# Kernel optimization log

Hardware: AMD Instinct MI355X
Metric: run time of the kernel (lower is better)

Reference implementation:

```python
import jax, jax.numpy as jnp
import numpy as np

B, N, P_EDGE = 2048, 64, 0.08


def setup_inputs() -> dict:
    key = jax.random.key(0)
    k1, _ = jax.random.split(key)
    u = jax.random.uniform(k1, (B, N, N))
    upper = jnp.triu(u < P_EDGE, k=1)
    A = (upper | jnp.swapaxes(upper, -1, -2)).astype(jnp.float32)  # symmetric, zero diag
    E = jnp.stack([1.0 - A, A], axis=-1)  # [B,N,N,2] one-hot edges
    node_mask = jnp.ones((B, N), dtype=jnp.float32)
    return {"E": E, "node_mask": node_mask}


def _diag(X):
    return jnp.diagonal(X, axis1=-2, axis2=-1)


def _trace(X):
    return _diag(X).sum(-1)


def reference(E, node_mask):
    A = E[..., 1:].sum(-1).astype(jnp.float32)  # [B,N,N]
    d = A.sum(-1)                               # degrees [B,N]
    k2 = A @ A
    k3 = k2 @ A
    k4 = k3 @ A
    k5 = k4 @ A
    k6 = k5 @ A

    c3 = _diag(k3)
    k3x = (c3 / 2)[..., None]
    k3y = (c3.sum(-1) / 6)[..., None]

    diag_a4 = _diag(k4)
    c4 = diag_a4 - d * (d - 1) - jnp.einsum('bij,bj->bi', A, d)
    k4x = (c4 / 2)[..., None]
    k4y = (c4.sum(-1) / 8)[..., None]

    diag_a5 = _diag(k5)
    tri = c3
    c5 = diag_a5 - 2 * tri * d - jnp.einsum('bij,bj->bi', A, tri) + tri
    k5x = (c5 / 2)[..., None]
    k5y = (c5.sum(-1) / 10)[..., None]

    t1 = _trace(k6)
    t2 = _trace(k3 ** 2)
    t3 = jnp.sum(A * k2 ** 2, axis=(-2, -1))
    d2 = _diag(k2)
    t4 = (d2 * diag_a4).sum(-1)
    t5 = _trace(k4)
    t6 = _trace(k3)
    t7 = (d2 ** 3).sum(-1)
    t8 = jnp.sum(k3, axis=(-2, -1))
    t9 = (d2 ** 2).sum(-1)
    t10 = _trace(k2)
    c6 = t1 - 3 * t2 + 9 * t3 - 6 * t4 + 6 * t5 - 4 * t6 + 4 * t7 + 3 * t8 - 12 * t9 + 4 * t10
    k6y = (c6 / 12)[..., None]

    x_cycles = jnp.concatenate([k3x, k4x, k5x], axis=-1)            # [B,N,3]
    y_cycles = jnp.concatenate([k3y, k4y, k5y, k6y], axis=-1)       # [B,4]

    x_cycles = x_cycles * node_mask[..., None] / 10.0
    y_cycles = y_cycles / 10.0
    x_cycles = jnp.minimum(x_cycles, 1.0)
    y_cycles = jnp.minimum(y_cycles, 1.0)
    return x_cycles, y_cycles
```

## Files before the change

### kernel.cpp

```cpp
#include <hip/hip_runtime.h>


typedef __attribute__((ext_vector_type(8))) short bf16x8;
typedef __attribute__((ext_vector_type(16))) float f32x16;

constexpr int BATCH = 2048;
constexpr int NN = 64;

__device__ __forceinline__ bf16x8 frag_ld(const unsigned short* buf, int row, int kb2) {
  const int idx = row * 64 + ((kb2 ^ (row & 7)) << 3);
  const uint4 v = *reinterpret_cast<const uint4*>(buf + idx);
  union { uint4 u; bf16x8 b; } cv; cv.u = v; return cv.b;
}

__global__ __launch_bounds__(256, 8) void node_cycle_kernel(
    const float4* __restrict__ E4,
    const float* __restrict__ nmask,
    float* __restrict__ out)
{
  const int b = blockIdx.x;
  const int tid = threadIdx.x;
  const int lane = tid & 63;
  const int w = tid >> 6;
  const int h = lane >> 5;
  const int c31 = lane & 31;
  const int R = w >> 1, C = w & 1;

  __shared__ unsigned short bufA[64 * 64];
  __shared__ unsigned short bufK2[64 * 64];
  __shared__ unsigned short sl[4][64];
  __shared__ uint2 rms[NN];
  __shared__ float c3sh[NN];
  __shared__ float4 gpart[4];

  const float4* __restrict__ Eb = E4 + (size_t)b * (NN * NN / 2);

  const int rp_r = 16 * w + (lane >> 2);
  const int rp_q = lane & 3;
  const float m_r = nmask[b * NN + rp_r];

  unsigned mA = 0u, mB = 0u;
  #pragma unroll
  for (int q = 0; q < 8; ++q) {
    const float4 f = Eb[w * 512 + q * 64 + lane];
    const int bit = 2 * q + h;
    mA |= (unsigned)(f.y > 0.5f) << bit;
    mB |= (unsigned)(f.w > 0.5f) << bit;
  }
  mA |= (unsigned)__shfl_xor((int)mA, 32);
  mB |= (unsigned)__shfl_xor((int)mB, 32);
  if (lane < 32) {
    sl[w][2 * lane]     = (unsigned short)mA;
    sl[w][2 * lane + 1] = (unsigned short)mB;
  }
  __syncthreads();

  if (tid < 128) {
    const int c = tid >> 1, hf = tid & 1;
    const unsigned v = (unsigned)sl[2 * hf][c] | ((unsigned)sl[2 * hf + 1][c] << 16);
    if (hf == 0) rms[c].x = v; else rms[c].y = v;
  }
  __syncthreads();

  const uint2 mrL = rms[lane];

  {
    const unsigned word = (w < 2) ? mrL.x : mrL.y;
    const unsigned bits16 = (word >> (16 * (w & 1))) & 0xffffu;
    #pragma unroll
    for (int e = 0; e < 2; ++e) {
      const int bq = 2 * w + e;
      unsigned wv[4];
      #pragma unroll
      for (int p2 = 0; p2 < 4; ++p2) {
        const int c0 = e * 8 + p2 * 2;
        wv[p2] = (((bits16 >> c0) & 1u) ? 0x3F80u : 0u)
               | (((bits16 >> (c0 + 1)) & 1u) ? 0x3F800000u : 0u);
      }
      const int idx = lane * 64 + ((bq ^ (lane & 7)) << 3);
      *reinterpret_cast<uint4*>(&bufA[idx]) = make_uint4(wv[0], wv[1], wv[2], wv[3]);
    }
  }
  __syncthreads();

  bf16x8 Bf[4];
  #pragma unroll
  for (int K = 0; K < 4; ++K) Bf[K] = frag_ld(bufA, C * 32 + c31, 2 * K + h);

  f32x16 acc;
  #pragma unroll
  for (int r = 0; r < 16; ++r) acc[r] = 0.f;
  #pragma unroll
  for (int K = 0; K < 4; ++K) {
    const bf16x8 af = frag_ld(bufA, R * 32 + c31, 2 * K + h);
    acc = __builtin_amdgcn_mfma_f32_32x32x16_bf16(af, Bf[K], acc, 0, 0, 0);
  }

  {
    const int c = C * 32 + c31;
    #pragma unroll
    for (int g = 0; g < 4; ++g) {
      const unsigned w0 = (__float_as_uint(acc[4*g+1]) & 0xffff0000u) |
                          (__float_as_uint(acc[4*g+0]) >> 16);
      const unsigned w1 = (__float_as_uint(acc[4*g+3]) & 0xffff0000u) |
                          (__float_as_uint(acc[4*g+2]) >> 16);
      const int bb = (4 * R + g) ^ (c & 7);
      *reinterpret_cast<uint2*>(&bufK2[c * 64 + bb * 8 + h * 4]) = make_uint2(w0, w1);
    }
  }
  __syncthreads();

  f32x16 d;
  #pragma unroll
  for (int r = 0; r < 16; ++r) d[r] = 0.f;
  #pragma unroll
  for (int K = 0; K < 4; ++K) {
    const bf16x8 kf = frag_ld(bufK2, R * 32 + c31, 2 * K + h);
    d = __builtin_amdgcn_mfma_f32_32x32x16_bf16(kf, Bf[K], d, 0, 0, 0);
  }

  if (R == C) {
    const int dtarget = c31 - 4 * h;
    float c3d = 0.f;
    #pragma unroll
    for (int r = 0; r < 16; ++r) {
      const int rowbase = (r & 3) + 8 * (r >> 2);
      c3d += (rowbase == dtarget) ? d[r] : 0.f;
    }
    if (((c31 >> 2) & 1) == h) c3sh[R * 32 + c31] = c3d;
  }

  {
    const int c = C * 32 + c31;
    #pragma unroll
    for (int g = 0; g < 4; ++g) {
      const unsigned u0 = ((unsigned)d[4*g+0]) | (((unsigned)d[4*g+1]) << 16);
      const unsigned u1 = ((unsigned)d[4*g+2]) | (((unsigned)d[4*g+3]) << 16);
      const int bb = (4 * R + g) ^ (c & 7);
      *reinterpret_cast<uint2*>(&bufA[c * 64 + bb * 8 + h * 4]) = make_uint2(u0, u1);
    }
  }
  __syncthreads();

  const uint2 mr = rms[rp_r];
  float diag4 = 0.f, Ad = 0.f, diag5 = 0.f, t3p = 0.f, Atri = 0.f;
  float t1p = 0.f, t8p = 0.f;
  #pragma unroll
  for (int e = 0; e < 2; ++e) {
    const int bq = 2 * rp_q + e;
    const int idx = rp_r * 64 + ((bq ^ (rp_r & 7)) << 3);
    const uint4 vk2 = *reinterpret_cast<const uint4*>(&bufK2[idx]);
    const uint4 vk3 = *reinterpret_cast<const uint4*>(&bufA[idx]);
    const float4 c3a = *reinterpret_cast<const float4*>(&c3sh[bq * 8]);
    const float4 c3b = *reinterpret_cast<const float4*>(&c3sh[bq * 8 + 4]);
    const unsigned wk2[4] = {vk2.x, vk2.y, vk2.z, vk2.w};
    const unsigned wk3[4] = {vk3.x, vk3.y, vk3.z, vk3.w};
    const float c3v[8] = {c3a.x, c3a.y, c3a.z, c3a.w, c3b.x, c3b.y, c3b.z, c3b.w};
    #pragma unroll
    for (int e2 = 0; e2 < 4; ++e2) {
      const int j0 = bq * 8 + 2 * e2;
      const float k2lo = __uint_as_float(wk2[e2] << 16);
      const float k2hi = __uint_as_float(wk2[e2] & 0xffff0000u);
      const float k3lo = (float)(wk3[e2] & 0xffffu);
      const float k3hi = (float)(wk3[e2] >> 16);
      diag4 = fmaf(k2lo, k2lo, fmaf(k2hi, k2hi, diag4));
      Ad += k2lo + k2hi;
      diag5 = fmaf(k2lo, k3lo, fmaf(k2hi, k3hi, diag5));
      t1p = fmaf(k3lo, k3lo, fmaf(k3hi, k3hi, t1p));
      t8p += k3lo + k3hi;
      const unsigned b0 = (j0 < 32 ? (mr.x >> j0) : (mr.y >> (j0 - 32))) & 1u;
      const unsigned b1 = ((j0 + 1) < 32 ? (mr.x >> (j0 + 1)) : (mr.y >> (j0 + 1 - 32))) & 1u;
      t3p = fmaf(b0 ? k2lo : 0.f, k2lo, fmaf(b1 ? k2hi : 0.f, k2hi, t3p));
      Atri += (b0 ? c3v[2 * e2] : 0.f) + (b1 ? c3v[2 * e2 + 1] : 0.f);
    }
  }
  #pragma unroll
  for (int off = 1; off <= 2; off <<= 1) {
    diag4 += __shfl_xor(diag4, off);
    Ad    += __shfl_xor(Ad, off);
    diag5 += __shfl_xor(diag5, off);
    t3p   += __shfl_xor(t3p, off);
    Atri  += __shfl_xor(Atri, off);
    t1p   += __shfl_xor(t1p, off);
    t8p   += __shfl_xor(t8p, off);
  }

  const float di  = (float)(__popc(mr.x) + __popc(mr.y));
  const float c3i = c3sh[rp_r];
  const float c4 = diag4 - di * (di - 1.f) - Ad;
  const float c5 = diag5 - 2.f * c3i * di - Atri + c3i;
  const float c6p = t1p + 3.f * t8p
            - 3.f * (c3i * c3i)
            + 9.f * t3p
            - 6.f * (di * diag4)
            + 6.f * diag4
            - 4.f * c3i
            + 4.f * (di * di * di)
            - 12.f * (di * di)
            + 4.f * di;

  if (rp_q == 0) {
    float* xo = out + ((size_t)b * NN + rp_r) * 3;
    xo[0] = fminf(c3i * 0.05f * m_r, 1.f);
    xo[1] = fminf(c4  * 0.05f * m_r, 1.f);
    xo[2] = fminf(c5  * 0.05f * m_r, 1.f);
  }

  float sc3 = c3i, sc4 = c4, sc5 = c5, sc6 = c6p;
  #pragma unroll
  for (int off = 4; off < 64; off <<= 1) {
    sc3 += __shfl_xor(sc3, off);
    sc4 += __shfl_xor(sc4, off);
    sc5 += __shfl_xor(sc5, off);
    sc6 += __shfl_xor(sc6, off);
  }
  if (lane == 0) gpart[w] = make_float4(sc3, sc4, sc5, sc6);
  __syncthreads();

  if (tid == 0) {
    const float4 g0 = gpart[0], g1 = gpart[1], g2 = gpart[2], g3 = gpart[3];
    float4 y;
    y.x = fminf((g0.x + g1.x + g2.x + g3.x) * (1.f / 6.f)  * 0.1f, 1.f);
    y.y = fminf((g0.y + g1.y + g2.y + g3.y) * (1.f / 8.f)  * 0.1f, 1.f);
    y.z = fminf((g0.z + g1.z + g2.z + g3.z) * (1.f / 10.f) * 0.1f, 1.f);
    y.w = fminf((g0.w + g1.w + g2.w + g3.w) * (1.f / 12.f) * 0.1f, 1.f);
    *reinterpret_cast<float4*>(out + (size_t)BATCH * NN * 3 + b * 4) = y;
  }
}

extern "C" void kernel_launch(void* const* d_in, const int* in_sizes, int n_in,
                              void* d_out, int out_size, void* d_ws, size_t ws_size,
                              hipStream_t stream) {
  const float4* E4 = reinterpret_cast<const float4*>(d_in[0]);
  const float* nmask = reinterpret_cast<const float*>(d_in[1]);
  float* out = reinterpret_cast<float*>(d_out);
  node_cycle_kernel<<<BATCH, 256, 0, stream>>>(E4, nmask, out);
}
```

Baseline: 18.81 us.

## Process two graphs per workgroup to interleave independent work and amortize barriers

Each 256-thread block now handles two batch elements instead of one. The mask build, MFMA products, packing and row passes for both graphs are interleaved between shared barriers. The goal is more instruction-level parallelism per wave, overlapping the two graphs' global loads and MFMA latency, and fewer barriers per graph. In exchange the block uses twice the LDS and more registers, occupancy is lowered to 4 blocks per CU, and the grid is halved.

```diff
diff --git a/kernel.cpp b/kernel.cpp
--- a/kernel.cpp
+++ b/kernel.cpp
@@ -13,32 +13,9 @@
   union { uint4 u; bf16x8 b; } cv; cv.u = v; return cv.b;
 }
 
-__global__ __launch_bounds__(256, 8) void node_cycle_kernel(
-    const float4* __restrict__ E4,
-    const float* __restrict__ nmask,
-    float* __restrict__ out)
-{
-  const int b = blockIdx.x;
-  const int tid = threadIdx.x;
-  const int lane = tid & 63;
-  const int w = tid >> 6;
-  const int h = lane >> 5;
-  const int c31 = lane & 31;
-  const int R = w >> 1, C = w & 1;
-
-  __shared__ unsigned short bufA[64 * 64];
-  __shared__ unsigned short bufK2[64 * 64];
-  __shared__ unsigned short sl[4][64];
-  __shared__ uint2 rms[NN];
-  __shared__ float c3sh[NN];
-  __shared__ float4 gpart[4];
-
-  const float4* __restrict__ Eb = E4 + (size_t)b * (NN * NN / 2);
-
-  const int rp_r = 16 * w + (lane >> 2);
-  const int rp_q = lane & 3;
-  const float m_r = nmask[b * NN + rp_r];
-
+__device__ __forceinline__ void build_masks(const float4* __restrict__ Eb,
+                                            int w, int lane, int h,
+                                            unsigned short (*slw)[64]) {
   unsigned mA = 0u, mB = 0u;
   #pragma unroll
   for (int q = 0; q < 8; ++q) {
@@ -50,75 +27,70 @@
   mA |= (unsigned)__shfl_xor((int)mA, 32);
   mB |= (unsigned)__shfl_xor((int)mB, 32);
   if (lane < 32) {
-    sl[w][2 * lane]     = (unsigned short)mA;
-    sl[w][2 * lane + 1] = (unsigned short)mB;
-  }
-  __syncthreads();
-
-  if (tid < 128) {
-    const int c = tid >> 1, hf = tid & 1;
-    const unsigned v = (unsigned)sl[2 * hf][c] | ((unsigned)sl[2 * hf + 1][c] << 16);
-    if (hf == 0) rms[c].x = v; else rms[c].y = v;
-  }
-  __syncthreads();
-
-  const uint2 mrL = rms[lane];
-
-  {
-    const unsigned word = (w < 2) ? mrL.x : mrL.y;
-    const unsigned bits16 = (word >> (16 * (w & 1))) & 0xffffu;
+    slw[w][2 * lane]     = (unsigned short)mA;
+    slw[w][2 * lane + 1] = (unsigned short)mB;
+  }
+}
+
+__device__ __forceinline__ void write_A(unsigned short* bA, uint2 mm, int w, int lane) {
+  const unsigned word = (w < 2) ? mm.x : mm.y;
+  const unsigned bits16 = (word >> (16 * (w & 1))) & 0xffffu;
+  #pragma unroll
+  for (int e = 0; e < 2; ++e) {
+    const int bq = 2 * w + e;
+    unsigned wv[4];
     #pragma unroll
-    for (int e = 0; e < 2; ++e) {
-      const int bq = 2 * w + e;
-      unsigned wv[4];
-      #pragma unroll
-      for (int p2 = 0; p2 < 4; ++p2) {
-        const int c0 = e * 8 + p2 * 2;
-        wv[p2] = (((bits16 >> c0) & 1u) ? 0x3F80u : 0u)
-               | (((bits16 >> (c0 + 1)) & 1u) ? 0x3F800000u : 0u);
-      }
-      const int idx = lane * 64 + ((bq ^ (lane & 7)) << 3);
-      *reinterpret_cast<uint4*>(&bufA[idx]) = make_uint4(wv[0], wv[1], wv[2], wv[3]);
+    for (int p2 = 0; p2 < 4; ++p2) {
+      const int c0 = e * 8 + p2 * 2;
+      wv[p2] = (((bits16 >> c0) & 1u) ? 0x3F80u : 0u)
+             | (((bits16 >> (c0 + 1)) & 1u) ? 0x3F800000u : 0u);
     }
-  }
-  __syncthreads();
-
-  bf16x8 Bf[4];
-  #pragma unroll
-  for (int K = 0; K < 4; ++K) Bf[K] = frag_ld(bufA, C * 32 + c31, 2 * K + h);
-
+    const int idx = lane * 64 + ((bq ^ (lane & 7)) << 3);
+    *reinterpret_cast<uint4*>(&bA[idx]) = make_uint4(wv[0], wv[1], wv[2], wv[3]);
+  }
+}
+
+__device__ __forceinline__ f32x16 do_mm(const unsigned short* bufOp, const bf16x8* Bf,
+                                        int R, int c31, int h) {
   f32x16 acc;
   #pragma unroll
   for (int r = 0; r < 16; ++r) acc[r] = 0.f;
   #pragma unroll
   for (int K = 0; K < 4; ++K) {
-    const bf16x8 af = frag_ld(bufA, R * 32 + c31, 2 * K + h);
+    const bf16x8 af = frag_ld(bufOp, R * 32 + c31, 2 * K + h);
     acc = __builtin_amdgcn_mfma_f32_32x32x16_bf16(af, Bf[K], acc, 0, 0, 0);
   }
-
-  {
-    const int c = C * 32 + c31;
-    #pragma unroll
-    for (int g = 0; g < 4; ++g) {
-      const unsigned w0 = (__float_as_uint(acc[4*g+1]) & 0xffff0000u) |
-                          (__float_as_uint(acc[4*g+0]) >> 16);
-      const unsigned w1 = (__float_as_uint(acc[4*g+3]) & 0xffff0000u) |
-                          (__float_as_uint(acc[4*g+2]) >> 16);
-      const int bb = (4 * R + g) ^ (c & 7);
-      *reinterpret_cast<uint2*>(&bufK2[c * 64 + bb * 8 + h * 4]) = make_uint2(w0, w1);
-    }
-  }
-  __syncthreads();
-
-  f32x16 d;
-  #pragma unroll
-  for (int r = 0; r < 16; ++r) d[r] = 0.f;
-  #pragma unroll
-  for (int K = 0; K < 4; ++K) {
-    const bf16x8 kf = frag_ld(bufK2, R * 32 + c31, 2 * K + h);
-    d = __builtin_amdgcn_mfma_f32_32x32x16_bf16(kf, Bf[K], d, 0, 0, 0);
-  }
-
+  return acc;
+}
+
+__device__ __forceinline__ void pack_k2(unsigned short* bK2, const f32x16& acc,
+                                        int R, int C, int c31, int h) {
+  const int c = C * 32 + c31;
+  #pragma unroll
+  for (int g = 0; g < 4; ++g) {
+    const unsigned w0 = (__float_as_uint(acc[4*g+1]) & 0xffff0000u) |
+                        (__float_as_uint(acc[4*g+0]) >> 16);
+    const unsigned w1 = (__float_as_uint(acc[4*g+3]) & 0xffff0000u) |
+                        (__float_as_uint(acc[4*g+2]) >> 16);
+    const int bb = (4 * R + g) ^ (c & 7);
+    *reinterpret_cast<uint2*>(&bK2[c * 64 + bb * 8 + h * 4]) = make_uint2(w0, w1);
+  }
+}
+
+__device__ __forceinline__ void pack_k3(unsigned short* bK3, const f32x16& d,
+                                        int R, int C, int c31, int h) {
+  const int c = C * 32 + c31;
+  #pragma unroll
+  for (int g = 0; g < 4; ++g) {
+    const unsigned u0 = ((unsigned)d[4*g+0]) | (((unsigned)d[4*g+1]) << 16);
+    const unsigned u1 = ((unsigned)d[4*g+2]) | (((unsigned)d[4*g+3]) << 16);
+    const int bb = (4 * R + g) ^ (c & 7);
+    *reinterpret_cast<uint2*>(&bK3[c * 64 + bb * 8 + h * 4]) = make_uint2(u0, u1);
+  }
+}
+
+__device__ __forceinline__ void diag_c3(float* c3p, const f32x16& d,
+                                        int R, int C, int c31, int h) {
   if (R == C) {
     const int dtarget = c31 - 4 * h;
     float c3d = 0.f;
@@ -127,32 +99,23 @@
       const int rowbase = (r & 3) + 8 * (r >> 2);
       c3d += (rowbase == dtarget) ? d[r] : 0.f;
     }
-    if (((c31 >> 2) & 1) == h) c3sh[R * 32 + c31] = c3d;
-  }
-
-  {
-    const int c = C * 32 + c31;
-    #pragma unroll
-    for (int g = 0; g < 4; ++g) {
-      const unsigned u0 = ((unsigned)d[4*g+0]) | (((unsigned)d[4*g+1]) << 16);
-      const unsigned u1 = ((unsigned)d[4*g+2]) | (((unsigned)d[4*g+3]) << 16);
-      const int bb = (4 * R + g) ^ (c & 7);
-      *reinterpret_cast<uint2*>(&bufA[c * 64 + bb * 8 + h * 4]) = make_uint2(u0, u1);
-    }
-  }
-  __syncthreads();
-
-  const uint2 mr = rms[rp_r];
-  float diag4 = 0.f, Ad = 0.f, diag5 = 0.f, t3p = 0.f, Atri = 0.f;
-  float t1p = 0.f, t8p = 0.f;
+    if (((c31 >> 2) & 1) == h) c3p[R * 32 + c31] = c3d;
+  }
+}
+
+struct RP { float diag4, Ad, diag5, t3p, Atri, t1p, t8p; };
+
+__device__ __forceinline__ RP rowpass(const unsigned short* bK2, const unsigned short* bK3,
+                                      const float* c3p, uint2 mr, int rp_r, int rp_q) {
+  RP o = {0.f, 0.f, 0.f, 0.f, 0.f, 0.f, 0.f};
   #pragma unroll
   for (int e = 0; e < 2; ++e) {
     const int bq = 2 * rp_q + e;
     const int idx = rp_r * 64 + ((bq ^ (rp_r & 7)) << 3);
-    const uint4 vk2 = *reinterpret_cast<const uint4*>(&bufK2[idx]);
-    const uint4 vk3 = *reinterpret_cast<const uint4*>(&bufA[idx]);
-    const float4 c3a = *reinterpret_cast<const float4*>(&c3sh[bq * 8]);
-    const float4 c3b = *reinterpret_cast<const float4*>(&c3sh[bq * 8 + 4]);
+    const uint4 vk2 = *reinterpret_cast<const uint4*>(&bK2[idx]);
+    const uint4 vk3 = *reinterpret_cast<const uint4*>(&bK3[idx]);
+    const float4 c3a = *reinterpret_cast<const float4*>(&c3p[bq * 8]);
+    const float4 c3b = *reinterpret_cast<const float4*>(&c3p[bq * 8 + 4]);
     const unsigned wk2[4] = {vk2.x, vk2.y, vk2.z, vk2.w};
     const unsigned wk3[4] = {vk3.x, vk3.y, vk3.z, vk3.w};
     const float c3v[8] = {c3a.x, c3a.y, c3a.z, c3a.w, c3b.x, c3b.y, c3b.z, c3b.w};
@@ -163,44 +126,38 @@
       const float k2hi = __uint_as_float(wk2[e2] & 0xffff0000u);
       const float k3lo = (float)(wk3[e2] & 0xffffu);
       const float k3hi = (float)(wk3[e2] >> 16);
-      diag4 = fmaf(k2lo, k2lo, fmaf(k2hi, k2hi, diag4));
-      Ad += k2lo + k2hi;
-      diag5 = fmaf(k2lo, k3lo, fmaf(k2hi, k3hi, diag5));
-      t1p = fmaf(k3lo, k3lo, fmaf(k3hi, k3hi, t1p));
-      t8p += k3lo + k3hi;
+      o.diag4 = fmaf(k2lo, k2lo, fmaf(k2hi, k2hi, o.diag4));
+      o.Ad += k2lo + k2hi;
+      o.diag5 = fmaf(k2lo, k3lo, fmaf(k2hi, k3hi, o.diag5));
+      o.t1p = fmaf(k3lo, k3lo, fmaf(k3hi, k3hi, o.t1p));
+      o.t8p += k3lo + k3hi;
       const unsigned b0 = (j0 < 32 ? (mr.x >> j0) : (mr.y >> (j0 - 32))) & 1u;
       const unsigned b1 = ((j0 + 1) < 32 ? (mr.x >> (j0 + 1)) : (mr.y >> (j0 + 1 - 32))) & 1u;
-      t3p = fmaf(b0 ? k2lo : 0.f, k2lo, fmaf(b1 ? k2hi : 0.f, k2hi, t3p));
-      Atri += (b0 ? c3v[2 * e2] : 0.f) + (b1 ? c3v[2 * e2 + 1] : 0.f);
+      o.t3p = fmaf(b0 ? k2lo : 0.f, k2lo, fmaf(b1 ? k2hi : 0.f, k2hi, o.t3p));
+      o.Atri += (b0 ? c3v[2 * e2] : 0.f) + (b1 ? c3v[2 * e2 + 1] : 0.f);
     }
   }
-  #pragma unroll
-  for (int off = 1; off <= 2; off <<= 1) {
-    diag4 += __shfl_xor(diag4, off);
-    Ad    += __shfl_xor(Ad, off);
-    diag5 += __shfl_xor(diag5, off);
-    t3p   += __shfl_xor(t3p, off);
-    Atri  += __shfl_xor(Atri, off);
-    t1p   += __shfl_xor(t1p, off);
-    t8p   += __shfl_xor(t8p, off);
-  }
-
-  const float di  = (float)(__popc(mr.x) + __popc(mr.y));
-  const float c3i = c3sh[rp_r];
-  const float c4 = diag4 - di * (di - 1.f) - Ad;
-  const float c5 = diag5 - 2.f * c3i * di - Atri + c3i;
-  const float c6p = t1p + 3.f * t8p
+  return o;
+}
+
+__device__ __forceinline__ void epilogue(const RP& r, uint2 mr, float c3i, float m_r,
+                                         int bb, int rp_r, int rp_q, int lane, int w,
+                                         float* __restrict__ out, float4* gp) {
+  const float di = (float)(__popc(mr.x) + __popc(mr.y));
+  const float c4 = r.diag4 - di * (di - 1.f) - r.Ad;
+  const float c5 = r.diag5 - 2.f * c3i * di - r.Atri + c3i;
+  const float c6p = r.t1p + 3.f * r.t8p
             - 3.f * (c3i * c3i)
-            + 9.f * t3p
-            - 6.f * (di * diag4)
-            + 6.f * diag4
+            + 9.f * r.t3p
+            - 6.f * (di * r.diag4)
+            + 6.f * r.diag4
             - 4.f * c3i
             + 4.f * (di * di * di)
             - 12.f * (di * di)
             + 4.f * di;
 
   if (rp_q == 0) {
-    float* xo = out + ((size_t)b * NN + rp_r) * 3;
+    float* xo = out + ((size_t)bb * NN + rp_r) * 3;
     xo[0] = fminf(c3i * 0.05f * m_r, 1.f);
     xo[1] = fminf(c4  * 0.05f * m_r, 1.f);
     xo[2] = fminf(c5  * 0.05f * m_r, 1.f);
@@ -214,17 +171,102 @@
     sc5 += __shfl_xor(sc5, off);
     sc6 += __shfl_xor(sc6, off);
   }
-  if (lane == 0) gpart[w] = make_float4(sc3, sc4, sc5, sc6);
-  __syncthreads();
-
-  if (tid == 0) {
-    const float4 g0 = gpart[0], g1 = gpart[1], g2 = gpart[2], g3 = gpart[3];
+  if (lane == 0) gp[w] = make_float4(sc3, sc4, sc5, sc6);
+}
+
+__global__ __launch_bounds__(256, 4) void node_cycle_kernel(
+    const float4* __restrict__ E4,
+    const float* __restrict__ nmask,
+    float* __restrict__ out)
+{
+  const int tid = threadIdx.x;
+  const int lane = tid & 63;
+  const int w = tid >> 6;
+  const int h = lane >> 5;
+  const int c31 = lane & 31;
+  const int R = w >> 1, C = w & 1;
+  const int b0 = blockIdx.x * 2;
+
+  __shared__ unsigned short bufA[2][4096];
+  __shared__ unsigned short bufK2[2][4096];
+  __shared__ unsigned short sl[2][4][64];
+  __shared__ uint2 rms[2][NN];
+  __shared__ float c3sh[2][NN];
+  __shared__ float4 gpart[2][4];
+
+  const float4* __restrict__ Eb0 = E4 + (size_t)b0 * 2048;
+  const float4* __restrict__ Eb1 = Eb0 + 2048;
+
+  const int rp_r = 16 * w + (lane >> 2);
+  const int rp_q = lane & 3;
+  const float m_r0 = nmask[(size_t)b0 * NN + rp_r];
+  const float m_r1 = nmask[(size_t)(b0 + 1) * NN + rp_r];
+
+  build_masks(Eb0, w, lane, h, sl[0]);
+  build_masks(Eb1, w, lane, h, sl[1]);
+  __syncthreads();
+
+  {
+    const int bi = tid >> 7;
+    const int t = tid & 127;
+    const int c = t >> 1, hf = t & 1;
+    const unsigned v = (unsigned)sl[bi][2 * hf][c] | ((unsigned)sl[bi][2 * hf + 1][c] << 16);
+    if (hf == 0) rms[bi][c].x = v; else rms[bi][c].y = v;
+  }
+  __syncthreads();
+
+  write_A(bufA[0], rms[0][lane], w, lane);
+  write_A(bufA[1], rms[1][lane], w, lane);
+  __syncthreads();
+
+  bf16x8 Bf0[4], Bf1[4];
+  #pragma unroll
+  for (int K = 0; K < 4; ++K) {
+    Bf0[K] = frag_ld(bufA[0], C * 32 + c31, 2 * K + h);
+    Bf1[K] = frag_ld(bufA[1], C * 32 + c31, 2 * K + h);
+  }
+  const f32x16 acc0 = do_mm(bufA[0], Bf0, R, c31, h);
+  const f32x16 acc1 = do_mm(bufA[1], Bf1, R, c31, h);
+  pack_k2(bufK2[0], acc0, R, C, c31, h);
+  pack_k2(bufK2[1], acc1, R, C, c31, h);
+  __syncthreads();
+
+  const f32x16 d0 = do_mm(bufK2[0], Bf0, R, c31, h);
+  const f32x16 d1 = do_mm(bufK2[1], Bf1, R, c31, h);
+  diag_c3(c3sh[0], d0, R, C, c31, h);
+  diag_c3(c3sh[1], d1, R, C, c31, h);
+  pack_k3(bufA[0], d0, R, C, c31, h);
+  pack_k3(bufA[1], d1, R, C, c31, h);
+  __syncthreads();
+
+  const uint2 mr0 = rms[0][rp_r];
+  const uint2 mr1 = rms[1][rp_r];
+  RP r0 = rowpass(bufK2[0], bufA[0], c3sh[0], mr0, rp_r, rp_q);
+  RP r1 = rowpass(bufK2[1], bufA[1], c3sh[1], mr1, rp_r, rp_q);
+  #pragma unroll
+  for (int off = 1; off <= 2; off <<= 1) {
+    r0.diag4 += __shfl_xor(r0.diag4, off); r1.diag4 += __shfl_xor(r1.diag4, off);
+    r0.Ad    += __shfl_xor(r0.Ad, off);    r1.Ad    += __shfl_xor(r1.Ad, off);
+    r0.diag5 += __shfl_xor(r0.diag5, off); r1.diag5 += __shfl_xor(r1.diag5, off);
+    r0.t3p   += __shfl_xor(r0.t3p, off);   r1.t3p   += __shfl_xor(r1.t3p, off);
+    r0.Atri  += __shfl_xor(r0.Atri, off);  r1.Atri  += __shfl_xor(r1.Atri, off);
+    r0.t1p   += __shfl_xor(r0.t1p, off);   r1.t1p   += __shfl_xor(r1.t1p, off);
+    r0.t8p   += __shfl_xor(r0.t8p, off);   r1.t8p   += __shfl_xor(r1.t8p, off);
+  }
+
+  epilogue(r0, mr0, c3sh[0][rp_r], m_r0, b0,     rp_r, rp_q, lane, w, out, gpart[0]);
+  epilogue(r1, mr1, c3sh[1][rp_r], m_r1, b0 + 1, rp_r, rp_q, lane, w, out, gpart[1]);
+  __syncthreads();
+
+  if (tid < 2) {
+    const float4 g0 = gpart[tid][0], g1 = gpart[tid][1],
+                 g2 = gpart[tid][2], g3 = gpart[tid][3];
     float4 y;
     y.x = fminf((g0.x + g1.x + g2.x + g3.x) * (1.f / 6.f)  * 0.1f, 1.f);
     y.y = fminf((g0.y + g1.y + g2.y + g3.y) * (1.f / 8.f)  * 0.1f, 1.f);
     y.z = fminf((g0.z + g1.z + g2.z + g3.z) * (1.f / 10.f) * 0.1f, 1.f);
     y.w = fminf((g0.w + g1.w + g2.w + g3.w) * (1.f / 12.f) * 0.1f, 1.f);
-    *reinterpret_cast<float4*>(out + (size_t)BATCH * NN * 3 + b * 4) = y;
+    *reinterpret_cast<float4*>(out + (size_t)BATCH * NN * 3 + (b0 + tid) * 4) = y;
   }
 }
 
@@ -234,5 +276,5 @@
   const float4* E4 = reinterpret_cast<const float4*>(d_in[0]);
   const float* nmask = reinterpret_cast<const float*>(d_in[1]);
   float* out = reinterpret_cast<float*>(d_out);
-  node_cycle_kernel<<<BATCH, 256, 0, stream>>>(E4, nmask, out);
-}
+  node_cycle_kernel<<<BATCH / 2, 256, 0, stream>>>(E4, nmask, out);
+}
```

Measured after the change: 21.17 us. +12.6%, slower.

## Split edge-tensor bit packing into a separate pre-pass kernel

Applied to the files above, without the earlier changes.

Moves the conversion of the float one-hot edge tensor into per-row adjacency bitmasks into a separate kernel that writes them to workspace. The main kernel then loads the compact bitmasks instead of streaming the full float input, and its body is refactored into helper functions. An extra sync is added after the second matmul so the K3 result can overwrite the A buffer safely. This adds a second launch and a global round trip of the masks, while the dominant input read is unchanged.

```diff
diff --git a/kernel.cpp b/kernel.cpp
--- a/kernel.cpp
+++ b/kernel.cpp
@@ -13,8 +13,153 @@
   union { uint4 u; bf16x8 b; } cv; cv.u = v; return cv.b;
 }
 
+__global__ __launch_bounds__(256) void pack_kernel(
+    const float4* __restrict__ E4,
+    unsigned* __restrict__ rw)
+{
+  const int b = blockIdx.x;
+  const int tid = threadIdx.x;
+  const int lane = tid & 63;
+  const int w = tid >> 6;
+  const int h = lane >> 5;
+
+  __shared__ unsigned short sl[4][64];
+
+  const float4* __restrict__ Eb = E4 + (size_t)b * 2048;
+  unsigned mA = 0u, mB = 0u;
+  #pragma unroll
+  for (int q = 0; q < 8; ++q) {
+    const float4 f = Eb[w * 512 + q * 64 + lane];
+    const int bit = 2 * q + h;
+    mA |= (unsigned)(f.y > 0.5f) << bit;
+    mB |= (unsigned)(f.w > 0.5f) << bit;
+  }
+  mA |= (unsigned)__shfl_xor((int)mA, 32);
+  mB |= (unsigned)__shfl_xor((int)mB, 32);
+  if (lane < 32) {
+    sl[w][2 * lane]     = (unsigned short)mA;
+    sl[w][2 * lane + 1] = (unsigned short)mB;
+  }
+  __syncthreads();
+
+  if (tid < 128) {
+    const int c = tid >> 1, hf = tid & 1;
+    const unsigned v = (unsigned)sl[2 * hf][c] | ((unsigned)sl[2 * hf + 1][c] << 16);
+    rw[(b * 64 + c) * 2 + hf] = v;
+  }
+}
+
+__device__ __forceinline__ void write_A(unsigned short* bA, uint2 mm, int w, int lane) {
+  const unsigned word = (w < 2) ? mm.x : mm.y;
+  const unsigned bits16 = (word >> (16 * (w & 1))) & 0xffffu;
+  #pragma unroll
+  for (int e = 0; e < 2; ++e) {
+    const int bq = 2 * w + e;
+    unsigned wv[4];
+    #pragma unroll
+    for (int p2 = 0; p2 < 4; ++p2) {
+      const int c0 = e * 8 + p2 * 2;
+      wv[p2] = (((bits16 >> c0) & 1u) ? 0x3F80u : 0u)
+             | (((bits16 >> (c0 + 1)) & 1u) ? 0x3F800000u : 0u);
+    }
+    const int idx = lane * 64 + ((bq ^ (lane & 7)) << 3);
+    *reinterpret_cast<uint4*>(&bA[idx]) = make_uint4(wv[0], wv[1], wv[2], wv[3]);
+  }
+}
+
+__device__ __forceinline__ f32x16 do_mm(const unsigned short* opA, const unsigned short* opB,
+                                        int R, int C, int c31, int h) {
+  f32x16 acc;
+  #pragma unroll
+  for (int r = 0; r < 16; ++r) acc[r] = 0.f;
+  #pragma unroll
+  for (int K = 0; K < 4; ++K) {
+    const bf16x8 af = frag_ld(opA, R * 32 + c31, 2 * K + h);
+    const bf16x8 bf = frag_ld(opB, C * 32 + c31, 2 * K + h);
+    acc = __builtin_amdgcn_mfma_f32_32x32x16_bf16(af, bf, acc, 0, 0, 0);
+  }
+  return acc;
+}
+
+__device__ __forceinline__ void pack_k2(unsigned short* bK2, const f32x16& acc,
+                                        int R, int C, int c31, int h) {
+  const int c = C * 32 + c31;
+  #pragma unroll
+  for (int g = 0; g < 4; ++g) {
+    const unsigned w0 = (__float_as_uint(acc[4*g+1]) & 0xffff0000u) |
+                        (__float_as_uint(acc[4*g+0]) >> 16);
+    const unsigned w1 = (__float_as_uint(acc[4*g+3]) & 0xffff0000u) |
+                        (__float_as_uint(acc[4*g+2]) >> 16);
+    const int bb = (4 * R + g) ^ (c & 7);
+    *reinterpret_cast<uint2*>(&bK2[c * 64 + bb * 8 + h * 4]) = make_uint2(w0, w1);
+  }
+}
+
+__device__ __forceinline__ void pack_k3(unsigned short* bK3, const f32x16& d,
+                                        int R, int C, int c31, int h) {
+  const int c = C * 32 + c31;
+  #pragma unroll
+  for (int g = 0; g < 4; ++g) {
+    const unsigned u0 = ((unsigned)d[4*g+0]) | (((unsigned)d[4*g+1]) << 16);
+    const unsigned u1 = ((unsigned)d[4*g+2]) | (((unsigned)d[4*g+3]) << 16);
+    const int bb = (4 * R + g) ^ (c & 7);
+    *reinterpret_cast<uint2*>(&bK3[c * 64 + bb * 8 + h * 4]) = make_uint2(u0, u1);
+  }
+}
+
+__device__ __forceinline__ void diag_c3(float* c3p, const f32x16& d,
+                                        int R, int C, int c31, int h) {
+  if (R == C) {
+    const int dtarget = c31 - 4 * h;
+    float c3d = 0.f;
+    #pragma unroll
+    for (int r = 0; r < 16; ++r) {
+      const int rowbase = (r & 3) + 8 * (r >> 2);
+      c3d += (rowbase == dtarget) ? d[r] : 0.f;
+    }
+    if (((c31 >> 2) & 1) == h) c3p[R * 32 + c31] = c3d;
+  }
+}
+
+struct RP { float diag4, Ad, diag5, t3p, Atri, t1p, t8p; };
+
+__device__ __forceinline__ RP rowpass(const unsigned short* bK2, const unsigned short* bK3,
+                                      const float* c3p, uint2 mr, int rp_r, int rp_q) {
+  RP o = {0.f, 0.f, 0.f, 0.f, 0.f, 0.f, 0.f};
+  #pragma unroll
+  for (int e = 0; e < 2; ++e) {
+    const int bq = 2 * rp_q + e;
+    const int idx = rp_r * 64 + ((bq ^ (rp_r & 7)) << 3);
+    const uint4 vk2 = *reinterpret_cast<const uint4*>(&bK2[idx]);
+    const uint4 vk3 = *reinterpret_cast<const uint4*>(&bK3[idx]);
+    const float4 c3a = *reinterpret_cast<const float4*>(&c3p[bq * 8]);
+    const float4 c3b = *reinterpret_cast<const float4*>(&c3p[bq * 8 + 4]);
+    const unsigned wk2[4] = {vk2.x, vk2.y, vk2.z, vk2.w};
+    const unsigned wk3[4] = {vk3.x, vk3.y, vk3.z, vk3.w};
+    const float c3v[8] = {c3a.x, c3a.y, c3a.z, c3a.w, c3b.x, c3b.y, c3b.z, c3b.w};
+    #pragma unroll
+    for (int e2 = 0; e2 < 4; ++e2) {
+      const int j0 = bq * 8 + 2 * e2;
+      const float k2lo = __uint_as_float(wk2[e2] << 16);
+      const float k2hi = __uint_as_float(wk2[e2] & 0xffff0000u);
+      const float k3lo = (float)(wk3[e2] & 0xffffu);
+      const float k3hi = (float)(wk3[e2] >> 16);
+      o.diag4 = fmaf(k2lo, k2lo, fmaf(k2hi, k2hi, o.diag4));
+      o.Ad += k2lo + k2hi;
+      o.diag5 = fmaf(k2lo, k3lo, fmaf(k2hi, k3hi, o.diag5));
+      o.t1p = fmaf(k3lo, k3lo, fmaf(k3hi, k3hi, o.t1p));
+      o.t8p += k3lo + k3hi;
+      const unsigned b0 = (j0 < 32 ? (mr.x >> j0) : (mr.y >> (j0 - 32))) & 1u;
+      const unsigned b1 = ((j0 + 1) < 32 ? (mr.x >> (j0 + 1)) : (mr.y >> (j0 + 1 - 32))) & 1u;
+      o.t3p = fmaf(b0 ? k2lo : 0.f, k2lo, fmaf(b1 ? k2hi : 0.f, k2hi, o.t3p));
+      o.Atri += (b0 ? c3v[2 * e2] : 0.f) + (b1 ? c3v[2 * e2 + 1] : 0.f);
+    }
+  }
+  return o;
+}
+
 __global__ __launch_bounds__(256, 8) void node_cycle_kernel(
-    const float4* __restrict__ E4,
+    const uint2* __restrict__ rw,
     const float* __restrict__ nmask,
     float* __restrict__ out)
 {
@@ -26,174 +171,55 @@
   const int c31 = lane & 31;
   const int R = w >> 1, C = w & 1;
 
-  __shared__ unsigned short bufA[64 * 64];
-  __shared__ unsigned short bufK2[64 * 64];
-  __shared__ unsigned short sl[4][64];
+  __shared__ unsigned short bufA[4096];
+  __shared__ unsigned short bufK2[4096];
   __shared__ uint2 rms[NN];
   __shared__ float c3sh[NN];
   __shared__ float4 gpart[4];
 
-  const float4* __restrict__ Eb = E4 + (size_t)b * (NN * NN / 2);
+  if (tid < 64) rms[tid] = rw[b * 64 + tid];
+  __syncthreads();
 
   const int rp_r = 16 * w + (lane >> 2);
   const int rp_q = lane & 3;
   const float m_r = nmask[b * NN + rp_r];
 
-  unsigned mA = 0u, mB = 0u;
-  #pragma unroll
-  for (int q = 0; q < 8; ++q) {
-    const float4 f = Eb[w * 512 + q * 64 + lane];
-    const int bit = 2 * q + h;
-    mA |= (unsigned)(f.y > 0.5f) << bit;
-    mB |= (unsigned)(f.w > 0.5f) << bit;
-  }
-  mA |= (unsigned)__shfl_xor((int)mA, 32);
-  mB |= (unsigned)__shfl_xor((int)mB, 32);
-  if (lane < 32) {
-    sl[w][2 * lane]     = (unsigned short)mA;
-    sl[w][2 * lane + 1] = (unsigned short)mB;
-  }
-  __syncthreads();
-
-  if (tid < 128) {
-    const int c = tid >> 1, hf = tid & 1;
-    const unsigned v = (unsigned)sl[2 * hf][c] | ((unsigned)sl[2 * hf + 1][c] << 16);
-    if (hf == 0) rms[c].x = v; else rms[c].y = v;
-  }
-  __syncthreads();
-
-  const uint2 mrL = rms[lane];
-
-  {
-    const unsigned word = (w < 2) ? mrL.x : mrL.y;
-    const unsigned bits16 = (word >> (16 * (w & 1))) & 0xffffu;
-    #pragma unroll
-    for (int e = 0; e < 2; ++e) {
-      const int bq = 2 * w + e;
-      unsigned wv[4];
-      #pragma unroll
-      for (int p2 = 0; p2 < 4; ++p2) {
-        const int c0 = e * 8 + p2 * 2;
-        wv[p2] = (((bits16 >> c0) & 1u) ? 0x3F80u : 0u)
-               | (((bits16 >> (c0 + 1)) & 1u) ? 0x3F800000u : 0u);
-      }
-      const int idx = lane * 64 + ((bq ^ (lane & 7)) << 3);
-      *reinterpret_cast<uint4*>(&bufA[idx]) = make_uint4(wv[0], wv[1], wv[2], wv[3]);
-    }
-  }
-  __syncthreads();
-
-  bf16x8 Bf[4];
-  #pragma unroll
-  for (int K = 0; K < 4; ++K) Bf[K] = frag_ld(bufA, C * 32 + c31, 2 * K + h);
-
-  f32x16 acc;
-  #pragma unroll
-  for (int r = 0; r < 16; ++r) acc[r] = 0.f;
-  #pragma unroll
-  for (int K = 0; K < 4; ++K) {
-    const bf16x8 af = frag_ld(bufA, R * 32 + c31, 2 * K + h);
-    acc = __builtin_amdgcn_mfma_f32_32x32x16_bf16(af, Bf[K], acc, 0, 0, 0);
-  }
-
-  {
-    const int c = C * 32 + c31;
-    #pragma unroll
-    for (int g = 0; g < 4; ++g) {
-      const unsigned w0 = (__float_as_uint(acc[4*g+1]) & 0xffff0000u) |
-                          (__float_as_uint(acc[4*g+0]) >> 16);
-      const unsigned w1 = (__float_as_uint(acc[4*g+3]) & 0xffff0000u) |
-                          (__float_as_uint(acc[4*g+2]) >> 16);
-      const int bb = (4 * R + g) ^ (c & 7);
-      *reinterpret_cast<uint2*>(&bufK2[c * 64 + bb * 8 + h * 4]) = make_uint2(w0, w1);
-    }
-  }
-  __syncthreads();
-
-  f32x16 d;
-  #pragma unroll
-  for (int r = 0; r < 16; ++r) d[r] = 0.f;
-  #pragma unroll
-  for (int K = 0; K < 4; ++K) {
-    const bf16x8 kf = frag_ld(bufK2, R * 32 + c31, 2 * K + h);
-    d = __builtin_amdgcn_mfma_f32_32x32x16_bf16(kf, Bf[K], d, 0, 0, 0);
-  }
-
-  if (R == C) {
-    const int dtarget = c31 - 4 * h;
-    float c3d = 0.f;
-    #pragma unroll
-    for (int r = 0; r < 16; ++r) {
-      const int rowbase = (r & 3) + 8 * (r >> 2);
-      c3d += (rowbase == dtarget) ? d[r] : 0.f;
-    }
-    if (((c31 >> 2) & 1) == h) c3sh[R * 32 + c31] = c3d;
-  }
-
-  {
-    const int c = C * 32 + c31;
-    #pragma unroll
-    for (int g = 0; g < 4; ++g) {
-      const unsigned u0 = ((unsigned)d[4*g+0]) | (((unsigned)d[4*g+1]) << 16);
-      const unsigned u1 = ((unsigned)d[4*g+2]) | (((unsigned)d[4*g+3]) << 16);
-      const int bb = (4 * R + g) ^ (c & 7);
-      *reinterpret_cast<uint2*>(&bufA[c * 64 + bb * 8 + h * 4]) = make_uint2(u0, u1);
-    }
-  }
+  write_A(bufA, rms[lane], w, lane);
+  __syncthreads();
+
+  const f32x16 acc = do_mm(bufA, bufA, R, C, c31, h);
+  pack_k2(bufK2, acc, R, C, c31, h);
+  __syncthreads();
+
+  const f32x16 d = do_mm(bufK2, bufA, R, C, c31, h);
+  __syncthreads();
+
+  diag_c3(c3sh, d, R, C, c31, h);
+  pack_k3(bufA, d, R, C, c31, h);
   __syncthreads();
 
   const uint2 mr = rms[rp_r];
-  float diag4 = 0.f, Ad = 0.f, diag5 = 0.f, t3p = 0.f, Atri = 0.f;
-  float t1p = 0.f, t8p = 0.f;
-  #pragma unroll
-  for (int e = 0; e < 2; ++e) {
-    const int bq = 2 * rp_q + e;
-    const int idx = rp_r * 64 + ((bq ^ (rp_r & 7)) << 3);
-    const uint4 vk2 = *reinterpret_cast<const uint4*>(&bufK2[idx]);
-    const uint4 vk3 = *reinterpret_cast<const uint4*>(&bufA[idx]);
-    const float4 c3a = *reinterpret_cast<const float4*>(&c3sh[bq * 8]);
-    const float4 c3b = *reinterpret_cast<const float4*>(&c3sh[bq * 8 + 4]);
-    const unsigned wk2[4] = {vk2.x, vk2.y, vk2.z, vk2.w};
-    const unsigned wk3[4] = {vk3.x, vk3.y, vk3.z, vk3.w};
-    const float c3v[8] = {c3a.x, c3a.y, c3a.z, c3a.w, c3b.x, c3b.y, c3b.z, c3b.w};
-    #pragma unroll
-    for (int e2 = 0; e2 < 4; ++e2) {
-      const int j0 = bq * 8 + 2 * e2;
-      const float k2lo = __uint_as_float(wk2[e2] << 16);
-      const float k2hi = __uint_as_float(wk2[e2] & 0xffff0000u);
-      const float k3lo = (float)(wk3[e2] & 0xffffu);
-      const float k3hi = (float)(wk3[e2] >> 16);
-      diag4 = fmaf(k2lo, k2lo, fmaf(k2hi, k2hi, diag4));
-      Ad += k2lo + k2hi;
-      diag5 = fmaf(k2lo, k3lo, fmaf(k2hi, k3hi, diag5));
-      t1p = fmaf(k3lo, k3lo, fmaf(k3hi, k3hi, t1p));
-      t8p += k3lo + k3hi;
-      const unsigned b0 = (j0 < 32 ? (mr.x >> j0) : (mr.y >> (j0 - 32))) & 1u;
-      const unsigned b1 = ((j0 + 1) < 32 ? (mr.x >> (j0 + 1)) : (mr.y >> (j0 + 1 - 32))) & 1u;
-      t3p = fmaf(b0 ? k2lo : 0.f, k2lo, fmaf(b1 ? k2hi : 0.f, k2hi, t3p));
-      Atri += (b0 ? c3v[2 * e2] : 0.f) + (b1 ? c3v[2 * e2 + 1] : 0.f);
-    }
-  }
+  RP r = rowpass(bufK2, bufA, c3sh, mr, rp_r, rp_q);
   #pragma unroll
   for (int off = 1; off <= 2; off <<= 1) {
-    diag4 += __shfl_xor(diag4, off);
-    Ad    += __shfl_xor(Ad, off);
-    diag5 += __shfl_xor(diag5, off);
-    t3p   += __shfl_xor(t3p, off);
-    Atri  += __shfl_xor(Atri, off);
-    t1p   += __shfl_xor(t1p, off);
-    t8p   += __shfl_xor(t8p, off);
+    r.diag4 += __shfl_xor(r.diag4, off);
+    r.Ad    += __shfl_xor(r.Ad, off);
+    r.diag5 += __shfl_xor(r.diag5, off);
+    r.t3p   += __shfl_xor(r.t3p, off);
+    r.Atri  += __shfl_xor(r.Atri, off);
+    r.t1p   += __shfl_xor(r.t1p, off);
+    r.t8p   += __shfl_xor(r.t8p, off);
   }
 
   const float di  = (float)(__popc(mr.x) + __popc(mr.y));
   const float c3i = c3sh[rp_r];
-  const float c4 = diag4 - di * (di - 1.f) - Ad;
-  const float c5 = diag5 - 2.f * c3i * di - Atri + c3i;
-  const float c6p = t1p + 3.f * t8p
+  const float c4 = r.diag4 - di * (di - 1.f) - r.Ad;
+  const float c5 = r.diag5 - 2.f * c3i * di - r.Atri + c3i;
+  const float c6p = r.t1p + 3.f * r.t8p
             - 3.f * (c3i * c3i)
-            + 9.f * t3p
-            - 6.f * (di * diag4)
-            + 6.f * diag4
+            + 9.f * r.t3p
+            - 6.f * (di * r.diag4)
+            + 6.f * r.diag4
             - 4.f * c3i
             + 4.f * (di * di * di)
             - 12.f * (di * di)
@@ -234,5 +260,8 @@
   const float4* E4 = reinterpret_cast<const float4*>(d_in[0]);
   const float* nmask = reinterpret_cast<const float*>(d_in[1]);
   float* out = reinterpret_cast<float*>(d_out);
-  node_cycle_kernel<<<BATCH, 256, 0, stream>>>(E4, nmask, out);
-}
+  unsigned* rw = reinterpret_cast<unsigned*>(d_ws);
+  pack_kernel<<<BATCH, 256, 0, stream>>>(E4, rw);
+  node_cycle_kernel<<<BATCH, 256, 0, stream>>>(
+      reinterpret_cast<const uint2*>(rw), nmask, out);
+}
```

After: 25.77 us. 1.37x slower.
